# Kernel optimization log

Hardware: AMD Instinct MI355X
Metric: run time of the kernel (lower is better)

## Reference

```python
import jax, jax.numpy as jnp
import numpy as np

IN_FEATURES = 4096
OUT_FEATURES = 4096
BATCH, SEQ = 4, 2048

def setup_inputs() -> dict:
    key = jax.random.key(0)
    k1, k2, k3, k4, k5 = jax.random.split(key, 5)
    x = jax.random.normal(k1, (BATCH, SEQ, IN_FEATURES), dtype=jnp.float32)
    # int8 codes stored as int32 in [0, 255] (asymmetric uint8-style quantization)
    qweight = jax.random.randint(k2, (OUT_FEATURES, IN_FEATURES), 0, 255, dtype=jnp.int32)
    scales = jax.random.uniform(k3, (OUT_FEATURES,), dtype=jnp.float32) * 0.01 + 1e-3
    zero_points = jax.random.uniform(k4, (OUT_FEATURES,), dtype=jnp.float32) * 255.0
    bias = jax.random.normal(k5, (OUT_FEATURES,), dtype=jnp.float32)
    return {"x": x, "qweight": qweight, "scales": scales, "zero_points": zero_points, "bias": bias}

def reference(x, qweight, scales, zero_points, bias):
    # Per-output-channel dequantization: W[o, i] = (q[o, i] - zp[o]) * scale[o]
    w = (qweight.astype(jnp.float32) - zero_points[:, None]) * scales[:, None]  # [O, I]
    # y = x @ W.T + b, fused dequant + GEMM in the original ipex op
    y = jnp.einsum("bsi,oi->bso", x, w) + bias
    return y
```

## Files before the change

kernel.cpp:

```cpp
#include <hip/hip_runtime.h>
#include <hip/hip_bf16.h>

typedef __attribute__((ext_vector_type(4))) int i32x4;
typedef __attribute__((ext_vector_type(16))) int i32x16;

#define M_DIM 8192
#define N_DIM 4096
#define K_DIM 4096
#define BM 256
#define BN 256
#define BK 128
#define NT2 (K_DIM / BK)

static __device__ inline void gload_lds16(const void* g, void* l) {
  __builtin_amdgcn_global_load_lds(
      (const __attribute__((address_space(1))) unsigned int*)g,
      (__attribute__((address_space(3))) unsigned int*)l,
      16, 0, 0);
}

__global__ __launch_bounds__(256) void prep_x_i8(
    const float* __restrict__ x, char* __restrict__ xq,
    float* __restrict__ rx, float* __restrict__ sxf) {
  const int row = blockIdx.x;
  const int tid = threadIdx.x;
  const float4* xr = (const float4*)(x + (long)row * K_DIM);
  float4 v[4];
  float mx = 0.f;
#pragma unroll
  for (int i = 0; i < 4; ++i) {
    v[i] = xr[i * 256 + tid];
    mx = fmaxf(mx, fmaxf(fmaxf(fabsf(v[i].x), fabsf(v[i].y)),
                         fmaxf(fabsf(v[i].z), fabsf(v[i].w))));
  }
#pragma unroll
  for (int off = 32; off > 0; off >>= 1) mx = fmaxf(mx, __shfl_down(mx, off, 64));
  __shared__ float redm[4];
  __shared__ int reds[4];
  const int lane = tid & 63, w = tid >> 6;
  if (lane == 0) redm[w] = mx;
  __syncthreads();
  const float maxv = fmaxf(fmaxf(redm[0], redm[1]), fmaxf(redm[2], redm[3]));
  const float inv = maxv > 0.f ? 127.f / maxv : 0.f;
  int* xo = (int*)(xq + (long)row * K_DIM);
  int ssum = 0;
#pragma unroll
  for (int i = 0; i < 4; ++i) {
    const int q0 = __float2int_rn(v[i].x * inv);
    const int q1 = __float2int_rn(v[i].y * inv);
    const int q2 = __float2int_rn(v[i].z * inv);
    const int q3 = __float2int_rn(v[i].w * inv);
    ssum += q0 + q1 + q2 + q3;
    xo[i * 256 + tid] =
        (q0 & 255) | ((q1 & 255) << 8) | ((q2 & 255) << 16) | ((q3 & 255) << 24);
  }
#pragma unroll
  for (int off = 32; off > 0; off >>= 1) ssum += __shfl_down(ssum, off, 64);
  if (lane == 0) reds[w] = ssum;
  __syncthreads();
  if (tid == 0) {
    rx[row] = maxv * (1.f / 127.f);
    sxf[row] = (float)(reds[0] + reds[1] + reds[2] + reds[3]);
  }
}

__global__ __launch_bounds__(256) void prep_q_i8(
    const int* __restrict__ q, char* __restrict__ qb) {
  const long idx = (long)blockIdx.x * blockDim.x + threadIdx.x;
  const int4 v = ((const int4*)q)[idx];
  const int a = v.x - 128, b = v.y - 128, c = v.z - 128, d = v.w - 128;
  ((int*)qb)[idx] = (a & 255) | ((b & 255) << 8) | ((c & 255) << 16) | ((d & 255) << 24);
}

__global__ __launch_bounds__(512, 2) void wq_gemm_i8(
    const char* __restrict__ A,
    const char* __restrict__ B,
    const float* __restrict__ rx,
    const float* __restrict__ sxf,
    const float* __restrict__ scales,
    const float* __restrict__ zps,
    const float* __restrict__ bias,
    float* __restrict__ C) {
  __shared__ __align__(16) char lds[2 * 65536];

  const int tid = threadIdx.x;
  const int lane = tid & 63;
  const int wv = tid >> 6;
  const int wr = wv >> 2, wc = wv & 3;

  const int wg = blockIdx.x;
  const int lid = (wg & 7) * 64 + (wg >> 3);
  const int bx = lid & 15, by = lid >> 4;
  const int brow = by * BM;
  const int bcol = bx * BN;

  i32x16 acc[4][2] = {};

  const int srow = tid >> 3;
  const int schunk = ((tid & 7) ^ (srow & 7)) * 16;
  const int wub = (tid & ~63) * 16;
  const char* gAs = A + (long)(brow + srow) * K_DIM + schunk;
  const char* gBs = B + (long)(bcol + srow) * K_DIM + schunk;

#define STAGE_A2(T, J0, J1)                                                   \
  do {                                                                        \
    char* d = lds + ((T) & 1) * 65536;                                        \
    gload_lds16(gAs + (long)(J0) * 262144 + (long)(T) * 128,                  \
                d + (J0) * 8192 + wub);                                       \
    gload_lds16(gAs + (long)(J1) * 262144 + (long)(T) * 128,                  \
                d + (J1) * 8192 + wub);                                       \
  } while (0)
#define STAGE_B2(T, J0, J1)                                                   \
  do {                                                                        \
    char* d = lds + ((T) & 1) * 65536 + 32768;                                \
    gload_lds16(gBs + (long)(J0) * 262144 + (long)(T) * 128,                  \
                d + (J0) * 8192 + wub);                                       \
    gload_lds16(gBs + (long)(J1) * 262144 + (long)(T) * 128,                  \
                d + (J1) * 8192 + wub);                                       \
  } while (0)

  const int row5 = lane & 31;
  const int kg = lane >> 5;
  int aoff[4];
#pragma unroll
  for (int ks = 0; ks < 4; ++ks) {
    const int ch = ((ks * 2 + kg) ^ (row5 & 7)) * 16;
    aoff[ks] = (wr * 128 + row5) * 128 + ch;
  }
  const int bdiff = (wc * 64 - wr * 128) * 128 + 32768;

#define RD_A(BB, FM, KS) (*(const i32x4*)(lds + (BB) + aoff[KS] + (FM) * 4096))
#define RD_B(BB, FN, KS) (*(const i32x4*)(lds + (BB) + aoff[KS] + bdiff + (FN) * 4096))
#define MMA(FM, FN, AV, BV)                                                   \
  acc[FM][FN] = __builtin_amdgcn_mfma_i32_32x32x32_i8(AV, BV, acc[FM][FN], 0, 0, 0)

#define BAR() __builtin_amdgcn_s_barrier()
#define VMC(N)                                                                \
  do {                                                                        \
    asm volatile("s_waitcnt vmcnt(" #N ")");                                  \
    __builtin_amdgcn_sched_barrier(0);                                        \
  } while (0)
#define LGK0()                                                                \
  do {                                                                        \
    asm volatile("s_waitcnt lgkmcnt(0)");                                     \
    __builtin_amdgcn_sched_barrier(0);                                        \
  } while (0)
#define SCHED() __builtin_amdgcn_sched_barrier(0)

  i32x4 fa00, fa01, fa02, fa03, fa10, fa11, fa12, fa13;
  i32x4 ga00, ga01, ga02, ga03, ga10, ga11, ga12, ga13;
  i32x4 vb00, vb01, vb02, vb03, vb10, vb11, vb12, vb13;

  STAGE_A2(0, 0, 2);
  STAGE_B2(0, 0, 2);
  STAGE_B2(0, 1, 3);
  STAGE_A2(0, 1, 3);
  VMC(2);
  BAR();
  fa00 = RD_A(0, 0, 0); fa01 = RD_A(0, 0, 1); fa02 = RD_A(0, 0, 2); fa03 = RD_A(0, 0, 3);
  fa10 = RD_A(0, 1, 0); fa11 = RD_A(0, 1, 1); fa12 = RD_A(0, 1, 2); fa13 = RD_A(0, 1, 3);
  vb00 = RD_B(0, 0, 0); vb01 = RD_B(0, 0, 1); vb02 = RD_B(0, 0, 2); vb03 = RD_B(0, 0, 3);
  vb10 = RD_B(0, 1, 0); vb11 = RD_B(0, 1, 1); vb12 = RD_B(0, 1, 2); vb13 = RD_B(0, 1, 3);

  for (int t = 0; t < NT2 - 1; ++t) {
    const int bb = (t & 1) * 65536;
    const int nb = bb ^ 65536;
    const int t1 = t + 1;
    STAGE_A2(t1, 0, 2);
    STAGE_B2(t1, 0, 2);
    STAGE_B2(t1, 1, 3);
    STAGE_A2(t1, 1, 3);
    VMC(8);
    BAR();
    ga00 = RD_A(bb, 2, 0); ga01 = RD_A(bb, 2, 1); ga02 = RD_A(bb, 2, 2); ga03 = RD_A(bb, 2, 3);
    ga10 = RD_A(bb, 3, 0); ga11 = RD_A(bb, 3, 1); ga12 = RD_A(bb, 3, 2); ga13 = RD_A(bb, 3, 3);
    SCHED();
    MMA(0, 0, fa00, vb00); MMA(0, 1, fa00, vb10);
    MMA(1, 0, fa10, vb00); MMA(1, 1, fa10, vb10);
    MMA(0, 0, fa01, vb01); MMA(0, 1, fa01, vb11);
    MMA(1, 0, fa11, vb01); MMA(1, 1, fa11, vb11);
    MMA(0, 0, fa02, vb02); MMA(0, 1, fa02, vb12);
    MMA(1, 0, fa12, vb02); MMA(1, 1, fa12, vb12);
    MMA(0, 0, fa03, vb03); MMA(0, 1, fa03, vb13);
    MMA(1, 0, fa13, vb03); MMA(1, 1, fa13, vb13);
    LGK0();
    VMC(2);
    BAR();
    fa00 = RD_A(nb, 0, 0); fa01 = RD_A(nb, 0, 1); fa02 = RD_A(nb, 0, 2); fa03 = RD_A(nb, 0, 3);
    fa10 = RD_A(nb, 1, 0); fa11 = RD_A(nb, 1, 1); fa12 = RD_A(nb, 1, 2); fa13 = RD_A(nb, 1, 3);
    SCHED();
    MMA(2, 0, ga00, vb00); MMA(2, 1, ga00, vb10);
    MMA(3, 0, ga10, vb00); MMA(3, 1, ga10, vb10);
    MMA(2, 0, ga01, vb01); MMA(2, 1, ga01, vb11);
    MMA(3, 0, ga11, vb01); MMA(3, 1, ga11, vb11);
    MMA(2, 0, ga02, vb02); MMA(2, 1, ga02, vb12);
    MMA(3, 0, ga12, vb02); MMA(3, 1, ga12, vb12);
    MMA(2, 0, ga03, vb03); MMA(2, 1, ga03, vb13);
    MMA(3, 0, ga13, vb03); MMA(3, 1, ga13, vb13);
    vb00 = RD_B(nb, 0, 0); vb01 = RD_B(nb, 0, 1); vb02 = RD_B(nb, 0, 2); vb03 = RD_B(nb, 0, 3);
    vb10 = RD_B(nb, 1, 0); vb11 = RD_B(nb, 1, 1); vb12 = RD_B(nb, 1, 2); vb13 = RD_B(nb, 1, 3);
  }

  {
    const int bb = 65536;
    VMC(0);
    BAR();
    ga00 = RD_A(bb, 2, 0); ga01 = RD_A(bb, 2, 1); ga02 = RD_A(bb, 2, 2); ga03 = RD_A(bb, 2, 3);
    ga10 = RD_A(bb, 3, 0); ga11 = RD_A(bb, 3, 1); ga12 = RD_A(bb, 3, 2); ga13 = RD_A(bb, 3, 3);
    SCHED();
    MMA(0, 0, fa00, vb00); MMA(0, 1, fa00, vb10);
    MMA(1, 0, fa10, vb00); MMA(1, 1, fa10, vb10);
    MMA(0, 0, fa01, vb01); MMA(0, 1, fa01, vb11);
    MMA(1, 0, fa11, vb01); MMA(1, 1, fa11, vb11);
    MMA(0, 0, fa02, vb02); MMA(0, 1, fa02, vb12);
    MMA(1, 0, fa12, vb02); MMA(1, 1, fa12, vb12);
    MMA(0, 0, fa03, vb03); MMA(0, 1, fa03, vb13);
    MMA(1, 0, fa13, vb03); MMA(1, 1, fa13, vb13);
    MMA(2, 0, ga00, vb00); MMA(2, 1, ga00, vb10);
    MMA(3, 0, ga10, vb00); MMA(3, 1, ga10, vb10);
    MMA(2, 0, ga01, vb01); MMA(2, 1, ga01, vb11);
    MMA(3, 0, ga11, vb01); MMA(3, 1, ga11, vb11);
    MMA(2, 0, ga02, vb02); MMA(2, 1, ga02, vb12);
    MMA(3, 0, ga12, vb02); MMA(3, 1, ga12, vb12);
    MMA(2, 0, ga03, vb03); MMA(2, 1, ga03, vb13);
    MMA(3, 0, ga13, vb03); MMA(3, 1, ga13, vb13);
  }

  float sc[2], zp[2], bs[2];
  int coln[2];
#pragma unroll
  for (int fn = 0; fn < 2; ++fn) {
    coln[fn] = bcol + wc * 64 + fn * 32 + row5;
    sc[fn] = scales[coln[fn]];
    zp[fn] = 128.f - zps[coln[fn]];
    bs[fn] = bias[coln[fn]];
  }
#pragma unroll
  for (int fm = 0; fm < 4; ++fm) {
#pragma unroll
    for (int r = 0; r < 16; ++r) {
      const int grow = brow + wr * 128 + fm * 32 + (r & 3) + 8 * (r >> 2) + 4 * kg;
      const float rxv = rx[grow];
      const float sxv = sxf[grow];
#pragma unroll
      for (int fn = 0; fn < 2; ++fn) {
        C[(long)grow * N_DIM + coln[fn]] =
            sc[fn] * rxv * ((float)acc[fm][fn][r] + zp[fn] * sxv) + bs[fn];
      }
    }
  }
}

extern "C" void kernel_launch(void* const* d_in, const int* in_sizes, int n_in,
                              void* d_out, int out_size, void* d_ws, size_t ws_size,
                              hipStream_t stream) {
  const float* x = (const float*)d_in[0];
  const int* qw = (const int*)d_in[1];
  const float* scales = (const float*)d_in[2];
  const float* zps = (const float*)d_in[3];
  const float* bias = (const float*)d_in[4];
  float* out = (float*)d_out;

  char* ws = (char*)d_ws;
  char* xq = ws;
  char* qb = ws + (size_t)32 * 1024 * 1024;
  float* rx = (float*)(ws + (size_t)48 * 1024 * 1024);
  float* sxf = (float*)(ws + (size_t)48 * 1024 * 1024 + 65536);

  hipLaunchKernelGGL(prep_x_i8, dim3(M_DIM), dim3(256), 0, stream, x, xq, rx, sxf);
  hipLaunchKernelGGL(prep_q_i8, dim3((N_DIM * K_DIM / 4) / 256), dim3(256), 0, stream,
                     qw, qb);
  hipLaunchKernelGGL(wq_gemm_i8, dim3((M_DIM / BM) * (N_DIM / BN)), dim3(512), 0,
                     stream, xq, qb, rx, sxf, scales, zps, bias, out);
}
```

Measured before the change: 194.9 us.

## Load B fragments directly from global into registers, stage only A in LDS

Weight (B) tiles are no longer staged through shared memory. Each wave now loads its B MFMA fragments straight from global memory into registers, one tile ahead, while only A goes through a smaller double-buffered LDS region. The main loop is rebuilt as a single-barrier-per-tile pipeline that alternates two register sets for B. This halves LDS usage and LDS traffic, which may allow higher occupancy. In exchange, B is fetched redundantly across waves through uncoalesced 16-byte global loads, and register pressure goes up.

```diff
diff --git a/kernel.cpp b/kernel.cpp
--- a/kernel.cpp
+++ b/kernel.cpp
@@ -81,7 +81,7 @@
     const float* __restrict__ zps,
     const float* __restrict__ bias,
     float* __restrict__ C) {
-  __shared__ __align__(16) char lds[2 * 65536];
+  __shared__ __align__(16) char lds[2 * 32768];
 
   const int tid = threadIdx.x;
   const int lane = tid & 63;
@@ -100,23 +100,14 @@
   const int schunk = ((tid & 7) ^ (srow & 7)) * 16;
   const int wub = (tid & ~63) * 16;
   const char* gAs = A + (long)(brow + srow) * K_DIM + schunk;
-  const char* gBs = B + (long)(bcol + srow) * K_DIM + schunk;
-
-#define STAGE_A2(T, J0, J1)                                                   \
-  do {                                                                        \
-    char* d = lds + ((T) & 1) * 65536;                                        \
-    gload_lds16(gAs + (long)(J0) * 262144 + (long)(T) * 128,                  \
-                d + (J0) * 8192 + wub);                                       \
-    gload_lds16(gAs + (long)(J1) * 262144 + (long)(T) * 128,                  \
-                d + (J1) * 8192 + wub);                                       \
-  } while (0)
-#define STAGE_B2(T, J0, J1)                                                   \
-  do {                                                                        \
-    char* d = lds + ((T) & 1) * 65536 + 32768;                                \
-    gload_lds16(gBs + (long)(J0) * 262144 + (long)(T) * 128,                  \
-                d + (J0) * 8192 + wub);                                       \
-    gload_lds16(gBs + (long)(J1) * 262144 + (long)(T) * 128,                  \
-                d + (J1) * 8192 + wub);                                       \
+
+#define STAGE_A4(T)                                                           \
+  do {                                                                        \
+    char* d = lds + ((T) & 1) * 32768;                                        \
+    gload_lds16(gAs + (long)(T) * 128, d + wub);                              \
+    gload_lds16(gAs + 262144 + (long)(T) * 128, d + 8192 + wub);              \
+    gload_lds16(gAs + 524288 + (long)(T) * 128, d + 16384 + wub);             \
+    gload_lds16(gAs + 786432 + (long)(T) * 128, d + 24576 + wub);             \
   } while (0)
 
   const int row5 = lane & 31;
@@ -127,10 +118,8 @@
     const int ch = ((ks * 2 + kg) ^ (row5 & 7)) * 16;
     aoff[ks] = (wr * 128 + row5) * 128 + ch;
   }
-  const int bdiff = (wc * 64 - wr * 128) * 128 + 32768;
 
 #define RD_A(BB, FM, KS) (*(const i32x4*)(lds + (BB) + aoff[KS] + (FM) * 4096))
-#define RD_B(BB, FN, KS) (*(const i32x4*)(lds + (BB) + aoff[KS] + bdiff + (FN) * 4096))
 #define MMA(FM, FN, AV, BV)                                                   \
   acc[FM][FN] = __builtin_amdgcn_mfma_i32_32x32x32_i8(AV, BV, acc[FM][FN], 0, 0, 0)
 
@@ -140,91 +129,76 @@
     asm volatile("s_waitcnt vmcnt(" #N ")");                                  \
     __builtin_amdgcn_sched_barrier(0);                                        \
   } while (0)
-#define LGK0()                                                                \
-  do {                                                                        \
-    asm volatile("s_waitcnt lgkmcnt(0)");                                     \
-    __builtin_amdgcn_sched_barrier(0);                                        \
-  } while (0)
 #define SCHED() __builtin_amdgcn_sched_barrier(0)
 
-  i32x4 fa00, fa01, fa02, fa03, fa10, fa11, fa12, fa13;
-  i32x4 ga00, ga01, ga02, ga03, ga10, ga11, ga12, ga13;
-  i32x4 vb00, vb01, vb02, vb03, vb10, vb11, vb12, vb13;
-
-  STAGE_A2(0, 0, 2);
-  STAGE_B2(0, 0, 2);
-  STAGE_B2(0, 1, 3);
-  STAGE_A2(0, 1, 3);
-  VMC(2);
+  const char* Bp = B + (long)(bcol + wc * 64 + row5) * K_DIM + kg * 16;
+
+  i32x4 u00, u01, u02, u03, u10, u11, u12, u13;
+  i32x4 w00, w01, w02, w03, w10, w11, w12, w13;
+
+#define LDB(S, T)                                                             \
+  do {                                                                        \
+    const char* bp = Bp + (long)(T) * 128;                                    \
+    S##00 = *(const i32x4*)(bp);                                              \
+    S##01 = *(const i32x4*)(bp + 32);                                         \
+    S##02 = *(const i32x4*)(bp + 64);                                         \
+    S##03 = *(const i32x4*)(bp + 96);                                         \
+    S##10 = *(const i32x4*)(bp + 131072);                                     \
+    S##11 = *(const i32x4*)(bp + 131072 + 32);                                \
+    S##12 = *(const i32x4*)(bp + 131072 + 64);                                \
+    S##13 = *(const i32x4*)(bp + 131072 + 96);                                \
+  } while (0)
+
+#define COMPUTE(BB, S)                                                        \
+  do {                                                                        \
+    i32x4 a0, a1, a2, a3;                                                     \
+    a0 = RD_A(BB, 0, 0); a1 = RD_A(BB, 0, 1); a2 = RD_A(BB, 0, 2); a3 = RD_A(BB, 0, 3); \
+    MMA(0, 0, a0, S##00); MMA(0, 1, a0, S##10);                               \
+    MMA(0, 0, a1, S##01); MMA(0, 1, a1, S##11);                               \
+    MMA(0, 0, a2, S##02); MMA(0, 1, a2, S##12);                               \
+    MMA(0, 0, a3, S##03); MMA(0, 1, a3, S##13);                               \
+    a0 = RD_A(BB, 1, 0); a1 = RD_A(BB, 1, 1); a2 = RD_A(BB, 1, 2); a3 = RD_A(BB, 1, 3); \
+    MMA(1, 0, a0, S##00); MMA(1, 1, a0, S##10);                               \
+    MMA(1, 0, a1, S##01); MMA(1, 1, a1, S##11);                               \
+    MMA(1, 0, a2, S##02); MMA(1, 1, a2, S##12);                               \
+    MMA(1, 0, a3, S##03); MMA(1, 1, a3, S##13);                               \
+    a0 = RD_A(BB, 2, 0); a1 = RD_A(BB, 2, 1); a2 = RD_A(BB, 2, 2); a3 = RD_A(BB, 2, 3); \
+    MMA(2, 0, a0, S##00); MMA(2, 1, a0, S##10);                               \
+    MMA(2, 0, a1, S##01); MMA(2, 1, a1, S##11);                               \
+    MMA(2, 0, a2, S##02); MMA(2, 1, a2, S##12);                               \
+    MMA(2, 0, a3, S##03); MMA(2, 1, a3, S##13);                               \
+    a0 = RD_A(BB, 3, 0); a1 = RD_A(BB, 3, 1); a2 = RD_A(BB, 3, 2); a3 = RD_A(BB, 3, 3); \
+    MMA(3, 0, a0, S##00); MMA(3, 1, a0, S##10);                               \
+    MMA(3, 0, a1, S##01); MMA(3, 1, a1, S##11);                               \
+    MMA(3, 0, a2, S##02); MMA(3, 1, a2, S##12);                               \
+    MMA(3, 0, a3, S##03); MMA(3, 1, a3, S##13);                               \
+  } while (0)
+
+#define TILE_BODY(T, CUR, NXT)                                                \
+  do {                                                                        \
+    const int bb_ = ((T) & 1) * 32768;                                        \
+    STAGE_A4((T) + 1);                                                        \
+    SCHED();                                                                  \
+    LDB(NXT, (T) + 1);                                                        \
+    SCHED();                                                                  \
+    COMPUTE(bb_, CUR);                                                        \
+    VMC(8);                                                                   \
+    BAR();                                                                    \
+  } while (0)
+
+  STAGE_A4(0);
+  SCHED();
+  LDB(u, 0);
+  SCHED();
+  VMC(8);
   BAR();
-  fa00 = RD_A(0, 0, 0); fa01 = RD_A(0, 0, 1); fa02 = RD_A(0, 0, 2); fa03 = RD_A(0, 0, 3);
-  fa10 = RD_A(0, 1, 0); fa11 = RD_A(0, 1, 1); fa12 = RD_A(0, 1, 2); fa13 = RD_A(0, 1, 3);
-  vb00 = RD_B(0, 0, 0); vb01 = RD_B(0, 0, 1); vb02 = RD_B(0, 0, 2); vb03 = RD_B(0, 0, 3);
-  vb10 = RD_B(0, 1, 0); vb11 = RD_B(0, 1, 1); vb12 = RD_B(0, 1, 2); vb13 = RD_B(0, 1, 3);
-
-  for (int t = 0; t < NT2 - 1; ++t) {
-    const int bb = (t & 1) * 65536;
-    const int nb = bb ^ 65536;
-    const int t1 = t + 1;
-    STAGE_A2(t1, 0, 2);
-    STAGE_B2(t1, 0, 2);
-    STAGE_B2(t1, 1, 3);
-    STAGE_A2(t1, 1, 3);
-    VMC(8);
-    BAR();
-    ga00 = RD_A(bb, 2, 0); ga01 = RD_A(bb, 2, 1); ga02 = RD_A(bb, 2, 2); ga03 = RD_A(bb, 2, 3);
-    ga10 = RD_A(bb, 3, 0); ga11 = RD_A(bb, 3, 1); ga12 = RD_A(bb, 3, 2); ga13 = RD_A(bb, 3, 3);
-    SCHED();
-    MMA(0, 0, fa00, vb00); MMA(0, 1, fa00, vb10);
-    MMA(1, 0, fa10, vb00); MMA(1, 1, fa10, vb10);
-    MMA(0, 0, fa01, vb01); MMA(0, 1, fa01, vb11);
-    MMA(1, 0, fa11, vb01); MMA(1, 1, fa11, vb11);
-    MMA(0, 0, fa02, vb02); MMA(0, 1, fa02, vb12);
-    MMA(1, 0, fa12, vb02); MMA(1, 1, fa12, vb12);
-    MMA(0, 0, fa03, vb03); MMA(0, 1, fa03, vb13);
-    MMA(1, 0, fa13, vb03); MMA(1, 1, fa13, vb13);
-    LGK0();
-    VMC(2);
-    BAR();
-    fa00 = RD_A(nb, 0, 0); fa01 = RD_A(nb, 0, 1); fa02 = RD_A(nb, 0, 2); fa03 = RD_A(nb, 0, 3);
-    fa10 = RD_A(nb, 1, 0); fa11 = RD_A(nb, 1, 1); fa12 = RD_A(nb, 1, 2); fa13 = RD_A(nb, 1, 3);
-    SCHED();
-    MMA(2, 0, ga00, vb00); MMA(2, 1, ga00, vb10);
-    MMA(3, 0, ga10, vb00); MMA(3, 1, ga10, vb10);
-    MMA(2, 0, ga01, vb01); MMA(2, 1, ga01, vb11);
-    MMA(3, 0, ga11, vb01); MMA(3, 1, ga11, vb11);
-    MMA(2, 0, ga02, vb02); MMA(2, 1, ga02, vb12);
-    MMA(3, 0, ga12, vb02); MMA(3, 1, ga12, vb12);
-    MMA(2, 0, ga03, vb03); MMA(2, 1, ga03, vb13);
-    MMA(3, 0, ga13, vb03); MMA(3, 1, ga13, vb13);
-    vb00 = RD_B(nb, 0, 0); vb01 = RD_B(nb, 0, 1); vb02 = RD_B(nb, 0, 2); vb03 = RD_B(nb, 0, 3);
-    vb10 = RD_B(nb, 1, 0); vb11 = RD_B(nb, 1, 1); vb12 = RD_B(nb, 1, 2); vb13 = RD_B(nb, 1, 3);
-  }
-
-  {
-    const int bb = 65536;
-    VMC(0);
-    BAR();
-    ga00 = RD_A(bb, 2, 0); ga01 = RD_A(bb, 2, 1); ga02 = RD_A(bb, 2, 2); ga03 = RD_A(bb, 2, 3);
-    ga10 = RD_A(bb, 3, 0); ga11 = RD_A(bb, 3, 1); ga12 = RD_A(bb, 3, 2); ga13 = RD_A(bb, 3, 3);
-    SCHED();
-    MMA(0, 0, fa00, vb00); MMA(0, 1, fa00, vb10);
-    MMA(1, 0, fa10, vb00); MMA(1, 1, fa10, vb10);
-    MMA(0, 0, fa01, vb01); MMA(0, 1, fa01, vb11);
-    MMA(1, 0, fa11, vb01); MMA(1, 1, fa11, vb11);
-    MMA(0, 0, fa02, vb02); MMA(0, 1, fa02, vb12);
-    MMA(1, 0, fa12, vb02); MMA(1, 1, fa12, vb12);
-    MMA(0, 0, fa03, vb03); MMA(0, 1, fa03, vb13);
-    MMA(1, 0, fa13, vb03); MMA(1, 1, fa13, vb13);
-    MMA(2, 0, ga00, vb00); MMA(2, 1, ga00, vb10);
-    MMA(3, 0, ga10, vb00); MMA(3, 1, ga10, vb10);
-    MMA(2, 0, ga01, vb01); MMA(2, 1, ga01, vb11);
-    MMA(3, 0, ga11, vb01); MMA(3, 1, ga11, vb11);
-    MMA(2, 0, ga02, vb02); MMA(2, 1, ga02, vb12);
-    MMA(3, 0, ga12, vb02); MMA(3, 1, ga12, vb12);
-    MMA(2, 0, ga03, vb03); MMA(2, 1, ga03, vb13);
-    MMA(3, 0, ga13, vb03); MMA(3, 1, ga13, vb13);
-  }
+
+  for (int tp = 0; tp < 15; ++tp) {
+    TILE_BODY(2 * tp, u, w);
+    TILE_BODY(2 * tp + 1, w, u);
+  }
+  TILE_BODY(30, u, w);
+  COMPUTE(32768, w);
 
   float sc[2], zp[2], bs[2];
   int coln[2];
```

After: 233.3 us. +19.7%, slower.

## Switch int8 GEMM to 16x16x64 MFMA with restructured half-tile LDS pipeline

Applied to the files above, without the earlier changes.

Replaces the 32x32x32 int8 MFMA with the 16x16x64 variant. Each wave's 128x64 tile becomes an 8x4 grid of 16x16 accumulators. The main loop now reads B fragments once per K-tile and runs the A rows in two halves of four fragments each, placing the next tile's staged loads and barriers between the halves. The aim is better MFMA throughput and a simpler, lower-latency LDS read schedule. The explicit lgkmcnt waits and sched barriers are removed, and the epilogue is remapped to the 16x16 accumulator layout.

```diff
diff --git a/kernel.cpp b/kernel.cpp
--- a/kernel.cpp
+++ b/kernel.cpp
@@ -2,7 +2,6 @@
 #include <hip/hip_bf16.h>
 
 typedef __attribute__((ext_vector_type(4))) int i32x4;
-typedef __attribute__((ext_vector_type(16))) int i32x16;
 
 #define M_DIM 8192
 #define N_DIM 4096
@@ -94,7 +93,7 @@
   const int brow = by * BM;
   const int bcol = bx * BN;
 
-  i32x16 acc[4][2] = {};
+  i32x4 acc[8][4] = {};
 
   const int srow = tid >> 3;
   const int schunk = ((tid & 7) ^ (srow & 7)) * 16;
@@ -119,20 +118,20 @@
                 d + (J1) * 8192 + wub);                                       \
   } while (0)
 
-  const int row5 = lane & 31;
-  const int kg = lane >> 5;
-  int aoff[4];
-#pragma unroll
-  for (int ks = 0; ks < 4; ++ks) {
-    const int ch = ((ks * 2 + kg) ^ (row5 & 7)) * 16;
-    aoff[ks] = (wr * 128 + row5) * 128 + ch;
-  }
-  const int bdiff = (wc * 64 - wr * 128) * 128 + 32768;
-
-#define RD_A(BB, FM, KS) (*(const i32x4*)(lds + (BB) + aoff[KS] + (FM) * 4096))
-#define RD_B(BB, FN, KS) (*(const i32x4*)(lds + (BB) + aoff[KS] + bdiff + (FN) * 4096))
+  const int row15 = lane & 15;
+  const int kq = lane >> 4;
+  int aoff[2], boff[2];
+#pragma unroll
+  for (int ks = 0; ks < 2; ++ks) {
+    const int ch = ((ks * 4 + kq) ^ (row15 & 7)) * 16;
+    aoff[ks] = (wr * 128 + row15) * 128 + ch;
+    boff[ks] = 32768 + (wc * 64 + row15) * 128 + ch;
+  }
+
+#define RD_A(BB, FM, KS) (*(const i32x4*)(lds + (BB) + aoff[KS] + (FM) * 2048))
+#define RD_B(BB, FN, KS) (*(const i32x4*)(lds + (BB) + boff[KS] + (FN) * 2048))
 #define MMA(FM, FN, AV, BV)                                                   \
-  acc[FM][FN] = __builtin_amdgcn_mfma_i32_32x32x32_i8(AV, BV, acc[FM][FN], 0, 0, 0)
+  acc[FM][FN] = __builtin_amdgcn_mfma_i32_16x16x64_i8(AV, BV, acc[FM][FN], 0, 0, 0)
 
 #define BAR() __builtin_amdgcn_s_barrier()
 #define VMC(N)                                                                \
@@ -140,16 +139,17 @@
     asm volatile("s_waitcnt vmcnt(" #N ")");                                  \
     __builtin_amdgcn_sched_barrier(0);                                        \
   } while (0)
-#define LGK0()                                                                \
-  do {                                                                        \
-    asm volatile("s_waitcnt lgkmcnt(0)");                                     \
-    __builtin_amdgcn_sched_barrier(0);                                        \
-  } while (0)
-#define SCHED() __builtin_amdgcn_sched_barrier(0)
-
-  i32x4 fa00, fa01, fa02, fa03, fa10, fa11, fa12, fa13;
-  i32x4 ga00, ga01, ga02, ga03, ga10, ga11, ga12, ga13;
-  i32x4 vb00, vb01, vb02, vb03, vb10, vb11, vb12, vb13;
+
+#define HALF_MMA(BB, FM0, AF, BF)                                             \
+  do {                                                                        \
+    _Pragma("unroll") for (int f = 0; f < 4; ++f)                             \
+      _Pragma("unroll") for (int ks = 0; ks < 2; ++ks)                        \
+        AF[f][ks] = RD_A(BB, (FM0) + f, ks);                                  \
+    _Pragma("unroll") for (int ks = 0; ks < 2; ++ks)                          \
+      _Pragma("unroll") for (int f = 0; f < 4; ++f)                           \
+        _Pragma("unroll") for (int n = 0; n < 4; ++n)                         \
+          MMA((FM0) + f, n, AF[f][ks], BF[n][ks]);                            \
+  } while (0)
 
   STAGE_A2(0, 0, 2);
   STAGE_B2(0, 0, 2);
@@ -157,95 +157,61 @@
   STAGE_A2(0, 1, 3);
   VMC(2);
   BAR();
-  fa00 = RD_A(0, 0, 0); fa01 = RD_A(0, 0, 1); fa02 = RD_A(0, 0, 2); fa03 = RD_A(0, 0, 3);
-  fa10 = RD_A(0, 1, 0); fa11 = RD_A(0, 1, 1); fa12 = RD_A(0, 1, 2); fa13 = RD_A(0, 1, 3);
-  vb00 = RD_B(0, 0, 0); vb01 = RD_B(0, 0, 1); vb02 = RD_B(0, 0, 2); vb03 = RD_B(0, 0, 3);
-  vb10 = RD_B(0, 1, 0); vb11 = RD_B(0, 1, 1); vb12 = RD_B(0, 1, 2); vb13 = RD_B(0, 1, 3);
+
+  i32x4 af[4][2], bf[4][2];
 
   for (int t = 0; t < NT2 - 1; ++t) {
     const int bb = (t & 1) * 65536;
-    const int nb = bb ^ 65536;
     const int t1 = t + 1;
+#pragma unroll
+    for (int n = 0; n < 4; ++n)
+#pragma unroll
+      for (int ks = 0; ks < 2; ++ks) bf[n][ks] = RD_B(bb, n, ks);
     STAGE_A2(t1, 0, 2);
     STAGE_B2(t1, 0, 2);
     STAGE_B2(t1, 1, 3);
+    HALF_MMA(bb, 0, af, bf);
+    VMC(6);
+    BAR();
     STAGE_A2(t1, 1, 3);
-    VMC(8);
-    BAR();
-    ga00 = RD_A(bb, 2, 0); ga01 = RD_A(bb, 2, 1); ga02 = RD_A(bb, 2, 2); ga03 = RD_A(bb, 2, 3);
-    ga10 = RD_A(bb, 3, 0); ga11 = RD_A(bb, 3, 1); ga12 = RD_A(bb, 3, 2); ga13 = RD_A(bb, 3, 3);
-    SCHED();
-    MMA(0, 0, fa00, vb00); MMA(0, 1, fa00, vb10);
-    MMA(1, 0, fa10, vb00); MMA(1, 1, fa10, vb10);
-    MMA(0, 0, fa01, vb01); MMA(0, 1, fa01, vb11);
-    MMA(1, 0, fa11, vb01); MMA(1, 1, fa11, vb11);
-    MMA(0, 0, fa02, vb02); MMA(0, 1, fa02, vb12);
-    MMA(1, 0, fa12, vb02); MMA(1, 1, fa12, vb12);
-    MMA(0, 0, fa03, vb03); MMA(0, 1, fa03, vb13);
-    MMA(1, 0, fa13, vb03); MMA(1, 1, fa13, vb13);
-    LGK0();
+    HALF_MMA(bb, 4, af, bf);
     VMC(2);
     BAR();
-    fa00 = RD_A(nb, 0, 0); fa01 = RD_A(nb, 0, 1); fa02 = RD_A(nb, 0, 2); fa03 = RD_A(nb, 0, 3);
-    fa10 = RD_A(nb, 1, 0); fa11 = RD_A(nb, 1, 1); fa12 = RD_A(nb, 1, 2); fa13 = RD_A(nb, 1, 3);
-    SCHED();
-    MMA(2, 0, ga00, vb00); MMA(2, 1, ga00, vb10);
-    MMA(3, 0, ga10, vb00); MMA(3, 1, ga10, vb10);
-    MMA(2, 0, ga01, vb01); MMA(2, 1, ga01, vb11);
-    MMA(3, 0, ga11, vb01); MMA(3, 1, ga11, vb11);
-    MMA(2, 0, ga02, vb02); MMA(2, 1, ga02, vb12);
-    MMA(3, 0, ga12, vb02); MMA(3, 1, ga12, vb12);
-    MMA(2, 0, ga03, vb03); MMA(2, 1, ga03, vb13);
-    MMA(3, 0, ga13, vb03); MMA(3, 1, ga13, vb13);
-    vb00 = RD_B(nb, 0, 0); vb01 = RD_B(nb, 0, 1); vb02 = RD_B(nb, 0, 2); vb03 = RD_B(nb, 0, 3);
-    vb10 = RD_B(nb, 1, 0); vb11 = RD_B(nb, 1, 1); vb12 = RD_B(nb, 1, 2); vb13 = RD_B(nb, 1, 3);
   }
 
   {
     const int bb = 65536;
+#pragma unroll
+    for (int n = 0; n < 4; ++n)
+#pragma unroll
+      for (int ks = 0; ks < 2; ++ks) bf[n][ks] = RD_B(bb, n, ks);
+    HALF_MMA(bb, 0, af, bf);
     VMC(0);
     BAR();
-    ga00 = RD_A(bb, 2, 0); ga01 = RD_A(bb, 2, 1); ga02 = RD_A(bb, 2, 2); ga03 = RD_A(bb, 2, 3);
-    ga10 = RD_A(bb, 3, 0); ga11 = RD_A(bb, 3, 1); ga12 = RD_A(bb, 3, 2); ga13 = RD_A(bb, 3, 3);
-    SCHED();
-    MMA(0, 0, fa00, vb00); MMA(0, 1, fa00, vb10);
-    MMA(1, 0, fa10, vb00); MMA(1, 1, fa10, vb10);
-    MMA(0, 0, fa01, vb01); MMA(0, 1, fa01, vb11);
-    MMA(1, 0, fa11, vb01); MMA(1, 1, fa11, vb11);
-    MMA(0, 0, fa02, vb02); MMA(0, 1, fa02, vb12);
-    MMA(1, 0, fa12, vb02); MMA(1, 1, fa12, vb12);
-    MMA(0, 0, fa03, vb03); MMA(0, 1, fa03, vb13);
-    MMA(1, 0, fa13, vb03); MMA(1, 1, fa13, vb13);
-    MMA(2, 0, ga00, vb00); MMA(2, 1, ga00, vb10);
-    MMA(3, 0, ga10, vb00); MMA(3, 1, ga10, vb10);
-    MMA(2, 0, ga01, vb01); MMA(2, 1, ga01, vb11);
-    MMA(3, 0, ga11, vb01); MMA(3, 1, ga11, vb11);
-    MMA(2, 0, ga02, vb02); MMA(2, 1, ga02, vb12);
-    MMA(3, 0, ga12, vb02); MMA(3, 1, ga12, vb12);
-    MMA(2, 0, ga03, vb03); MMA(2, 1, ga03, vb13);
-    MMA(3, 0, ga13, vb03); MMA(3, 1, ga13, vb13);
-  }
-
-  float sc[2], zp[2], bs[2];
-  int coln[2];
-#pragma unroll
-  for (int fn = 0; fn < 2; ++fn) {
-    coln[fn] = bcol + wc * 64 + fn * 32 + row5;
+    HALF_MMA(bb, 4, af, bf);
+  }
+
+  float sc[4], zp[4], bs[4];
+  int coln[4];
+#pragma unroll
+  for (int fn = 0; fn < 4; ++fn) {
+    coln[fn] = bcol + wc * 64 + fn * 16 + row15;
     sc[fn] = scales[coln[fn]];
     zp[fn] = 128.f - zps[coln[fn]];
     bs[fn] = bias[coln[fn]];
   }
 #pragma unroll
-  for (int fm = 0; fm < 4; ++fm) {
-#pragma unroll
-    for (int r = 0; r < 16; ++r) {
-      const int grow = brow + wr * 128 + fm * 32 + (r & 3) + 8 * (r >> 2) + 4 * kg;
+  for (int fm = 0; fm < 8; ++fm) {
+    const int r0 = brow + wr * 128 + fm * 16 + kq * 4;
+#pragma unroll
+    for (int j = 0; j < 4; ++j) {
+      const int grow = r0 + j;
       const float rxv = rx[grow];
       const float sxv = sxf[grow];
 #pragma unroll
-      for (int fn = 0; fn < 2; ++fn) {
+      for (int fn = 0; fn < 4; ++fn) {
         C[(long)grow * N_DIM + coln[fn]] =
-            sc[fn] * rxv * ((float)acc[fm][fn][r] + zp[fn] * sxv) + bs[fn];
+            sc[fn] * rxv * ((float)acc[fm][fn][j] + zp[fn] * sxv) + bs[fn];
       }
     }
   }
```

Result: faster. 179.8 us (median of 3 runs) (-7.7%).
